# Performance work log

Measured on AMD Instinct MI355X. Metric: run time of the kernel, lower is better.

The kernel has to match this reference:

```python
import jax, jax.numpy as jnp
import numpy as np

N_NODES = 50000
N_EDGES = 800000
F_IN = 256
HID = 64
HEADS = 4
NEG_SLOPE = 0.2


def setup_inputs() -> dict:
    key = jax.random.key(0)
    ks = jax.random.split(key, 12)
    x = jax.random.normal(ks[0], (N_NODES, F_IN), dtype=jnp.float32)
    src = jax.random.randint(ks[1], (N_EDGES,), 0, N_NODES)
    dst = jax.random.randint(ks[2], (N_EDGES,), 0, N_NODES)
    s0 = 1.0 / np.sqrt(F_IN)
    s1 = 1.0 / np.sqrt(HEADS * HID)
    W0 = jax.random.normal(ks[3], (F_IN, HEADS * HID), dtype=jnp.float32) * s0
    a_l0 = jax.random.normal(ks[4], (HEADS, HID), dtype=jnp.float32) * s1
    a_r0 = jax.random.normal(ks[5], (HEADS, HID), dtype=jnp.float32) * s1
    b0 = jnp.zeros((HEADS * HID,), dtype=jnp.float32)
    W1 = jax.random.normal(ks[6], (HEADS * HID, HEADS * HID), dtype=jnp.float32) * s1
    a_l1 = jax.random.normal(ks[7], (HEADS, HID), dtype=jnp.float32) * s1
    a_r1 = jax.random.normal(ks[8], (HEADS, HID), dtype=jnp.float32) * s1
    b1 = jnp.zeros((HEADS * HID,), dtype=jnp.float32)
    return {"x": x, "src": src, "dst": dst,
            "W0": W0, "a_l0": a_l0, "a_r0": a_r0, "b0": b0,
            "W1": W1, "a_l1": a_l1, "a_r1": a_r1, "b1": b1}


def _gat_layer(h, src, dst, W, a_l, a_r, b):
    # h: [N, F_in] -> feat: [N, H, D]
    feat = (h @ W).reshape(h.shape[0], HEADS, HID)
    el = jnp.sum(feat * a_l, axis=-1)  # [N, H]
    er = jnp.sum(feat * a_r, axis=-1)  # [N, H]
    e = jax.nn.leaky_relu(el[src] + er[dst], NEG_SLOPE)  # [E, H]
    # per-destination edge softmax (numerically stable)
    m = jax.ops.segment_max(e, dst, num_segments=N_NODES)  # [N, H]
    ex = jnp.exp(e - m[dst])
    s = jax.ops.segment_sum(ex, dst, num_segments=N_NODES)  # [N, H]
    alpha = ex / jnp.maximum(s[dst], 1e-9)  # [E, H]
    msg = feat[src] * alpha[:, :, None]  # [E, H, D]
    rst = jax.ops.segment_sum(msg, dst, num_segments=N_NODES)  # [N, H, D]
    rst = rst + b.reshape(1, HEADS, HID)
    return jax.nn.elu(rst)


def reference(x, src, dst, W0, a_l0, a_r0, b0, W1, a_l1, a_r1, b1):
    h = _gat_layer(x, src, dst, W0, a_l0, a_r0, b0)  # [N, H, D]
    h = h.reshape(N_NODES, HEADS * HID)              # flatten(1)
    h = _gat_layer(h, src, dst, W1, a_l1, a_r1, b1)  # [N, H, D]
    # list of per-head outputs h[:, i]
    return tuple(h[:, i] for i in range(HEADS))
```

## Files before the change

kernel.cpp:

```cpp
#include <hip/hip_runtime.h>
#include <math.h>

#define N_NODES 50000
#define N_EDGES 800000
#define HEADS 4
#define HID 64
#define FDIM 256
#define SCAN_CHUNK 1024
#define SCAN_NB ((N_NODES + SCAN_CHUNK - 1) / SCAN_CHUNK)

typedef __attribute__((ext_vector_type(8))) _Float16 half8;
typedef __attribute__((ext_vector_type(4))) _Float16 half4;
typedef __attribute__((ext_vector_type(4))) float f32x4;

__device__ __forceinline__ void gload_lds16(const void* g, void* l) {
    __builtin_amdgcn_global_load_lds((const __attribute__((address_space(1))) void*)g,
                                     (__attribute__((address_space(3))) void*)l, 16, 0, 0);
}


__global__ __launch_bounds__(256) void scan_local(const int* __restrict__ counts,
                                                  int* __restrict__ offs,
                                                  int* __restrict__ bsum, int n) {
    __shared__ int part[256];
    const int b = blockIdx.x, t = threadIdx.x;
    const int base = b * SCAN_CHUNK + t * 4;
    int v[4];
#pragma unroll
    for (int j = 0; j < 4; j++) {
        int idx = base + j;
        v[j] = (idx < n) ? counts[idx] : 0;
    }
    int s0 = v[0], s1 = s0 + v[1], s2 = s1 + v[2], s3 = s2 + v[3];
    part[t] = s3;
    __syncthreads();
    for (int off = 1; off < 256; off <<= 1) {
        int x = (t >= off) ? part[t - off] : 0;
        __syncthreads();
        part[t] += x;
        __syncthreads();
    }
    int prefix = (t > 0) ? part[t - 1] : 0;
    int e[4] = {prefix, prefix + s0, prefix + s1, prefix + s2};
#pragma unroll
    for (int j = 0; j < 4; j++) {
        int idx = base + j;
        if (idx < n) offs[idx] = e[j];
    }
    if (t == 255) bsum[b] = part[255];
}

__global__ __launch_bounds__(64) void scan_bsum(int* __restrict__ bsum,
                                                int* __restrict__ offs, int nb, int n) {
    int lane = threadIdx.x;
    int own = (lane < nb) ? bsum[lane] : 0;
    int v = own;
    for (int off = 1; off < 64; off <<= 1) {
        int x = __shfl_up(v, off);
        if (lane >= off) v += x;
    }
    if (lane < nb) bsum[lane] = v - own;
    if (lane == nb - 1) offs[n] = v;
}

__global__ __launch_bounds__(256) void scan_add(int* __restrict__ offs,
                                                const int* __restrict__ bsum, int n) {
    const int b = blockIdx.x;
    const int p = bsum[b];
    const int base = b * SCAN_CHUNK + threadIdx.x * 4;
#pragma unroll
    for (int j = 0; j < 4; j++) {
        int idx = base + j;
        if (idx < n) offs[idx] += p;
    }
}

__global__ __launch_bounds__(256) void scatter_kernel(const int* __restrict__ src,
                                                      const int* __restrict__ dst,
                                                      const int* __restrict__ offs,
                                                      const int* __restrict__ rank,
                                                      int* __restrict__ csr_src, int E) {
    int i = blockIdx.x * blockDim.x + threadIdx.x;
    if (i < E) {
        int d = dst[i];
        csr_src[offs[d] + rank[i]] = src[i];
    }
}


__global__ __launch_bounds__(256) void wcast_kernel(const float* __restrict__ W0,
                                                    const float* __restrict__ W1,
                                                    _Float16* __restrict__ wt0,
                                                    _Float16* __restrict__ wt1) {
    const float* W = blockIdx.y ? W1 : W0;
    _Float16* wt = blockIdx.y ? wt1 : wt0;
    int n = blockIdx.x * 16 + (threadIdx.x >> 4);
    int k0 = (threadIdx.x & 15) * 16;
    for (int j = 0; j < 16; j++)
        wt[n * FDIM + k0 + j] = (_Float16)W[(k0 + j) * FDIM + n];
}

template <int A32, int DO_HIST>
__global__ __launch_bounds__(512) void mfma_gemm(const _Float16* __restrict__ A16,
                                                 const float* __restrict__ Af,
                                                 const _Float16* __restrict__ Bt,
                                                 const float* __restrict__ al,
                                                 const float* __restrict__ ar,
                                                 _Float16* __restrict__ feat16,
                                                 float* __restrict__ el,
                                                 float* __restrict__ er,
                                                 const int* __restrict__ dst,
                                                 int* __restrict__ counts,
                                                 int* __restrict__ rank) {
    __shared__ _Float16 ash[2][64 * 32];
    __shared__ _Float16 bsh[2][256 * 32];

    const int t = threadIdx.x;
    const int m0 = blockIdx.x * 64;
    const int wave = t >> 6, lane = t & 63;
    const int quad = lane >> 4, l16 = lane & 15;
    const int wr = (wave >> 2) * 32;
    const int wc = (wave & 3) * 64;

    const int arow = t >> 3, aq4 = t & 7;
    const int agr = (m0 + arow < N_NODES) ? m0 + arow : N_NODES - 1;
    const int aswz = (aq4 >> 1) ^ (arow & 3) ^ ((arow >> 2) & 3);
    const int aoff = arow * 32 + aswz * 8 + (aq4 & 1) * 4;

    const f32x4 zero = {0.f, 0.f, 0.f, 0.f};
    f32x4 acc[2][4];
#pragma unroll
    for (int i = 0; i < 2; i++)
#pragma unroll
        for (int j = 0; j < 4; j++) acc[i][j] = zero;

    const int rslot = (quad ^ (l16 & 3) ^ (l16 >> 2)) * 8;

    float4 areg;

    if (A32) {
        const float* p = &Af[(size_t)agr * FDIM + aq4 * 4];
        float4 f0 = *(const float4*)p;
        half4 hv = {(_Float16)f0.x, (_Float16)f0.y, (_Float16)f0.z, (_Float16)f0.w};
        *(half4*)&ash[0][aoff] = hv;
    } else {
        if (wave < 4) {
            int u = wave * 64 + lane;
            int row = u >> 2, sl = u & 3;
            int ss = sl ^ (row & 3) ^ ((row >> 2) & 3);
            int gr = (m0 + row < N_NODES) ? m0 + row : N_NODES - 1;
            gload_lds16(&A16[(size_t)gr * FDIM + ss * 8], &ash[0][u * 8]);
        }
    }
#pragma unroll
    for (int ii = 0; ii < 2; ii++) {
        int u = (wave * 2 + ii) * 64 + lane;
        int row = u >> 2, sl = u & 3;
        int ss = sl ^ (row & 3) ^ ((row >> 2) & 3);
        gload_lds16(&Bt[(size_t)row * FDIM + ss * 8], &bsh[0][u * 8]);
    }
    __syncthreads();

    for (int ks = 0; ks < 8; ks++) {
        const int cur = ks & 1, nxt = cur ^ 1;
        const int kk2 = (ks + 1) * 32;
        const bool pf = (ks < 7);

        if (pf) {
            if (A32) {
                areg = *(const float4*)&Af[(size_t)agr * FDIM + kk2 + aq4 * 4];
            } else {
                if (wave < 4) {
                    int u = wave * 64 + lane;
                    int row = u >> 2, sl = u & 3;
                    int ss = sl ^ (row & 3) ^ ((row >> 2) & 3);
                    int gr = (m0 + row < N_NODES) ? m0 + row : N_NODES - 1;
                    gload_lds16(&A16[(size_t)gr * FDIM + kk2 + ss * 8], &ash[nxt][u * 8]);
                }
            }
#pragma unroll
            for (int ii = 0; ii < 2; ii++) {
                int u = (wave * 2 + ii) * 64 + lane;
                int row = u >> 2, sl = u & 3;
                int ss = sl ^ (row & 3) ^ ((row >> 2) & 3);
                gload_lds16(&Bt[(size_t)row * FDIM + kk2 + ss * 8], &bsh[nxt][u * 8]);
            }
        }

        half8 af[2], bf[4];
#pragma unroll
        for (int i = 0; i < 2; i++)
            af[i] = *(half8*)&ash[cur][(wr + i * 16 + l16) * 32 + rslot];
#pragma unroll
        for (int i = 0; i < 4; i++)
            bf[i] = *(half8*)&bsh[cur][(wc + i * 16 + l16) * 32 + rslot];

#pragma unroll
        for (int mt = 0; mt < 2; mt++)
#pragma unroll
            for (int nt = 0; nt < 4; nt++)
                acc[mt][nt] = __builtin_amdgcn_mfma_f32_16x16x32_f16(bf[nt], af[mt], acc[mt][nt], 0, 0, 0);

        if (A32 && pf) {
            half4 hv = {(_Float16)areg.x, (_Float16)areg.y, (_Float16)areg.z, (_Float16)areg.w};
            *(half4*)&ash[nxt][aoff] = hv;
        }
        if (pf) __syncthreads();
    }

    if (DO_HIST) {
        for (int i = blockIdx.x * 512 + t; i < N_EDGES; i += gridDim.x * 512)
            rank[i] = atomicAdd(&counts[dst[i]], 1);
    }

    const int h = wc >> 6;
    float4 alv[4], arv[4];
#pragma unroll
    for (int nt = 0; nt < 4; nt++) {
        alv[nt] = *(const float4*)&al[wc + nt * 16 + quad * 4];
        arv[nt] = *(const float4*)&ar[wc + nt * 16 + quad * 4];
    }
#pragma unroll
    for (int mt = 0; mt < 2; mt++) {
        const int m = m0 + wr + mt * 16 + l16;
        const bool ok = (m < N_NODES);
        float pl = 0.f, pr = 0.f;
#pragma unroll
        for (int nt = 0; nt < 4; nt++) {
            f32x4 v = acc[mt][nt];
            if (ok) {
                half4 hv = {(_Float16)v[0], (_Float16)v[1], (_Float16)v[2], (_Float16)v[3]};
                *(half4*)&feat16[(size_t)m * FDIM + wc + nt * 16 + quad * 4] = hv;
            }
            pl += v[0] * alv[nt].x + v[1] * alv[nt].y + v[2] * alv[nt].z + v[3] * alv[nt].w;
            pr += v[0] * arv[nt].x + v[1] * arv[nt].y + v[2] * arv[nt].z + v[3] * arv[nt].w;
        }
        pl += __shfl_xor(pl, 16);
        pl += __shfl_xor(pl, 32);
        pr += __shfl_xor(pr, 16);
        pr += __shfl_xor(pr, 32);
        if (quad == 0 && ok) {
            el[m * 4 + h] = pl;
            er[m * 4 + h] = pr;
        }
    }
}

__global__ __launch_bounds__(256) void agg_fused(const _Float16* __restrict__ feat16,
                                                 const float* __restrict__ el,
                                                 const float* __restrict__ er,
                                                 const float* __restrict__ bias,
                                                 const int* __restrict__ offs,
                                                 const int* __restrict__ csr_src,
                                                 float* __restrict__ out,
                                                 _Float16* __restrict__ h1,
                                                 int mode) {
    const int wave = threadIdx.x >> 6;
    const int lane = threadIdx.x & 63;
    const int n = blockIdx.x * 4 + wave;
    const int head = lane >> 4;
    const int f = lane * 4;
    const int base16 = lane & 48;
    const int j16 = lane & 15;
    const int beg = offs[n];
    const int end = offs[n + 1];
    const float er_h = er[n * 4 + head];

    float4 acc = make_float4(0.f, 0.f, 0.f, 0.f);
    float ss = 0.f;

    for (int c = beg; c < end; c += 16) {
        int e = c + j16;
        int s_own = 0;
        float w_own = 0.f;
        if (e < end) {
            s_own = csr_src[e];
            float lg = el[s_own * 4 + head] + er_h;
            lg = (lg > 0.f) ? lg : 0.2f * lg;
            w_own = __expf(lg);
        }
        ss += w_own;

        int rem = end - c;
        if (rem > 16) rem = 16;

        int j = 0;
        for (; j + 3 < rem; j += 4) {
            int s0 = __shfl(s_own, base16 + j);
            int s1 = __shfl(s_own, base16 + j + 1);
            int s2 = __shfl(s_own, base16 + j + 2);
            int s3 = __shfl(s_own, base16 + j + 3);
            float w0 = __shfl(w_own, base16 + j);
            float w1 = __shfl(w_own, base16 + j + 1);
            float w2 = __shfl(w_own, base16 + j + 2);
            float w3 = __shfl(w_own, base16 + j + 3);
            half4 v0 = *(const half4*)&feat16[(size_t)s0 * FDIM + f];
            half4 v1 = *(const half4*)&feat16[(size_t)s1 * FDIM + f];
            half4 v2 = *(const half4*)&feat16[(size_t)s2 * FDIM + f];
            half4 v3 = *(const half4*)&feat16[(size_t)s3 * FDIM + f];
            acc.x += w0 * (float)v0[0] + w1 * (float)v1[0];
            acc.y += w0 * (float)v0[1] + w1 * (float)v1[1];
            acc.z += w0 * (float)v0[2] + w1 * (float)v1[2];
            acc.w += w0 * (float)v0[3] + w1 * (float)v1[3];
            acc.x += w2 * (float)v2[0] + w3 * (float)v3[0];
            acc.y += w2 * (float)v2[1] + w3 * (float)v3[1];
            acc.z += w2 * (float)v2[2] + w3 * (float)v3[2];
            acc.w += w2 * (float)v2[3] + w3 * (float)v3[3];
        }
        for (; j < rem; j++) {
            int s0 = __shfl(s_own, base16 + j);
            float w0 = __shfl(w_own, base16 + j);
            half4 v0 = *(const half4*)&feat16[(size_t)s0 * FDIM + f];
            acc.x += w0 * (float)v0[0];
            acc.y += w0 * (float)v0[1];
            acc.z += w0 * (float)v0[2];
            acc.w += w0 * (float)v0[3];
        }
    }

    ss += __shfl_xor(ss, 1, 16);
    ss += __shfl_xor(ss, 2, 16);
    ss += __shfl_xor(ss, 4, 16);
    ss += __shfl_xor(ss, 8, 16);

    float S = fmaxf(ss, 1e-9f);
    float inv = 1.f / S;
    float4 bv = *(const float4*)&bias[f];
    float r0 = acc.x * inv + bv.x;
    float r1 = acc.y * inv + bv.y;
    float r2 = acc.z * inv + bv.z;
    float r3 = acc.w * inv + bv.w;
    r0 = (r0 > 0.f) ? r0 : expm1f(r0);
    r1 = (r1 > 0.f) ? r1 : expm1f(r1);
    r2 = (r2 > 0.f) ? r2 : expm1f(r2);
    r3 = (r3 > 0.f) ? r3 : expm1f(r3);

    if (mode) {
        const int d = (lane & 15) * 4;
        float4 rv = make_float4(r0, r1, r2, r3);
        *(float4*)&out[(size_t)head * N_NODES * HID + (size_t)n * HID + d] = rv;
    } else {
        half4 hv = {(_Float16)r0, (_Float16)r1, (_Float16)r2, (_Float16)r3};
        *(half4*)&h1[(size_t)n * FDIM + f] = hv;
    }
}


extern "C" void kernel_launch(void* const* d_in, const int* in_sizes, int n_in,
                              void* d_out, int out_size, void* d_ws, size_t ws_size,
                              hipStream_t stream) {
    const float* x   = (const float*)d_in[0];
    const int*   src = (const int*)d_in[1];
    const int*   dst = (const int*)d_in[2];
    const float* W0  = (const float*)d_in[3];
    const float* al0 = (const float*)d_in[4];
    const float* ar0 = (const float*)d_in[5];
    const float* b0  = (const float*)d_in[6];
    const float* W1  = (const float*)d_in[7];
    const float* al1 = (const float*)d_in[8];
    const float* ar1 = (const float*)d_in[9];
    const float* b1  = (const float*)d_in[10];
    float* out = (float*)d_out;

    _Float16* h1 = (_Float16*)d_out;

    _Float16* feat16 = (_Float16*)d_ws;
    _Float16* wt0 = feat16 + (size_t)N_NODES * FDIM;
    _Float16* wt1 = wt0 + FDIM * FDIM;
    float* el    = (float*)(wt1 + FDIM * FDIM);
    float* er    = el + N_NODES * HEADS;
    int* counts  = (int*)(er + N_NODES * HEADS);
    int* offs    = counts + N_NODES;
    int* bsum    = offs + 50016;
    int* csr_src = bsum + 64;
    int* rank    = csr_src + N_EDGES;

    const int ggrid = (N_NODES + 63) / 64;

    hipMemsetAsync(counts, 0, N_NODES * sizeof(int), stream);
    wcast_kernel<<<dim3(16, 2), 256, 0, stream>>>(W0, W1, wt0, wt1);

    mfma_gemm<1, 1><<<ggrid, 512, 0, stream>>>(nullptr, x, wt0, al0, ar0,
                                               feat16, el, er, dst, counts, rank);

    scan_local<<<SCAN_NB, 256, 0, stream>>>(counts, offs, bsum, N_NODES);
    scan_bsum<<<1, 64, 0, stream>>>(bsum, offs, SCAN_NB, N_NODES);
    scan_add<<<SCAN_NB, 256, 0, stream>>>(offs, bsum, N_NODES);
    scatter_kernel<<<(N_EDGES + 255) / 256, 256, 0, stream>>>(src, dst, offs, rank, csr_src, N_EDGES);

    agg_fused<<<N_NODES / 4, 256, 0, stream>>>(feat16, el, er, b0, offs, csr_src,
                                               out, h1, 0);

    mfma_gemm<0, 0><<<ggrid, 512, 0, stream>>>(h1, nullptr, wt1, al1, ar1,
                                               feat16, el, er, nullptr, nullptr, nullptr);
    agg_fused<<<N_NODES / 4, 256, 0, stream>>>(feat16, el, er, b1, offs, csr_src,
                                               out, h1, 1);
}
```

Baseline: 343.7 us.

## Fuse weight cast with counter zeroing and use single-pass decoupled lookback scan

```diff
diff --git a/kernel.cpp b/kernel.cpp
--- a/kernel.cpp
+++ b/kernel.cpp
@@ -18,11 +18,36 @@
                                      (__attribute__((address_space(3))) void*)l, 16, 0, 0);
 }
 
-
-__global__ __launch_bounds__(256) void scan_local(const int* __restrict__ counts,
-                                                  int* __restrict__ offs,
-                                                  int* __restrict__ bsum, int n) {
+__global__ __launch_bounds__(256) void prep_kernel(const float* __restrict__ W0,
+                                                   const float* __restrict__ W1,
+                                                   _Float16* __restrict__ wt0,
+                                                   _Float16* __restrict__ wt1,
+                                                   int* __restrict__ counts,
+                                                   int* __restrict__ flags) {
+    const int b = blockIdx.x, t = threadIdx.x;
+    if (b < 32) {
+        const float* W = (b >= 16) ? W1 : W0;
+        _Float16* wt = (b >= 16) ? wt1 : wt0;
+        int n = (b & 15) * 16 + (t >> 4);
+        int k0 = (t & 15) * 16;
+        for (int j = 0; j < 16; j++)
+            wt[n * FDIM + k0 + j] = (_Float16)W[(k0 + j) * FDIM + n];
+    } else {
+        int4 z = make_int4(0, 0, 0, 0);
+        int4* p = (int4*)counts;
+        for (int k = (b - 32) * 256 + t; k < N_NODES / 4; k += 13 * 256)
+            p[k] = z;
+        if (b == 32 && t < 64) flags[t] = 0;
+    }
+}
+
+__global__ __launch_bounds__(256) void scan_lookback(const int* __restrict__ counts,
+                                                     int* __restrict__ offs,
+                                                     int* __restrict__ aggv,
+                                                     int* __restrict__ prefv,
+                                                     int* __restrict__ flags, int n) {
     __shared__ int part[256];
+    __shared__ int sh_exc;
     const int b = blockIdx.x, t = threadIdx.x;
     const int base = b * SCAN_CHUNK + t * 4;
     int v[4];
@@ -40,39 +65,40 @@
         part[t] += x;
         __syncthreads();
     }
-    int prefix = (t > 0) ? part[t - 1] : 0;
+    const int total = part[255];
+
+    if (t == 0) {
+        atomicExch(&aggv[b], total);
+        __threadfence();
+        atomicExch(&flags[b], 1);
+    }
+    if (t < 64) {
+        int p = b - 1 - t;
+        int f = 2, a = 0;
+        if (p >= 0) {
+            do { f = atomicAdd(&flags[p], 0); } while (f == 0);
+            a = (f == 2) ? atomicAdd(&prefv[p], 0) : atomicAdd(&aggv[p], 0);
+        }
+        unsigned long long m = __ballot(f == 2);
+        int t2 = __ffsll((long long)m) - 1;
+        int contrib = (t <= t2) ? a : 0;
+        for (int off = 32; off; off >>= 1) contrib += __shfl_down(contrib, off);
+        if (t == 0) {
+            atomicExch(&prefv[b], contrib + total);
+            __threadfence();
+            atomicExch(&flags[b], 2);
+            sh_exc = contrib;
+        }
+    }
+    __syncthreads();
+    const int prefix = sh_exc + ((t > 0) ? part[t - 1] : 0);
     int e[4] = {prefix, prefix + s0, prefix + s1, prefix + s2};
 #pragma unroll
     for (int j = 0; j < 4; j++) {
         int idx = base + j;
         if (idx < n) offs[idx] = e[j];
     }
-    if (t == 255) bsum[b] = part[255];
-}
-
-__global__ __launch_bounds__(64) void scan_bsum(int* __restrict__ bsum,
-                                                int* __restrict__ offs, int nb, int n) {
-    int lane = threadIdx.x;
-    int own = (lane < nb) ? bsum[lane] : 0;
-    int v = own;
-    for (int off = 1; off < 64; off <<= 1) {
-        int x = __shfl_up(v, off);
-        if (lane >= off) v += x;
-    }
-    if (lane < nb) bsum[lane] = v - own;
-    if (lane == nb - 1) offs[n] = v;
-}
-
-__global__ __launch_bounds__(256) void scan_add(int* __restrict__ offs,
-                                                const int* __restrict__ bsum, int n) {
-    const int b = blockIdx.x;
-    const int p = bsum[b];
-    const int base = b * SCAN_CHUNK + threadIdx.x * 4;
-#pragma unroll
-    for (int j = 0; j < 4; j++) {
-        int idx = base + j;
-        if (idx < n) offs[idx] += p;
-    }
+    if (b == (int)gridDim.x - 1 && t == 255) offs[n] = sh_exc + total;
 }
 
 __global__ __launch_bounds__(256) void scatter_kernel(const int* __restrict__ src,
@@ -85,19 +111,6 @@
         int d = dst[i];
         csr_src[offs[d] + rank[i]] = src[i];
     }
-}
-
-
-__global__ __launch_bounds__(256) void wcast_kernel(const float* __restrict__ W0,
-                                                    const float* __restrict__ W1,
-                                                    _Float16* __restrict__ wt0,
-                                                    _Float16* __restrict__ wt1) {
-    const float* W = blockIdx.y ? W1 : W0;
-    _Float16* wt = blockIdx.y ? wt1 : wt0;
-    int n = blockIdx.x * 16 + (threadIdx.x >> 4);
-    int k0 = (threadIdx.x & 15) * 16;
-    for (int j = 0; j < 16; j++)
-        wt[n * FDIM + k0 + j] = (_Float16)W[(k0 + j) * FDIM + n];
 }
 
 template <int A32, int DO_HIST>
@@ -371,21 +384,20 @@
     float* er    = el + N_NODES * HEADS;
     int* counts  = (int*)(er + N_NODES * HEADS);
     int* offs    = counts + N_NODES;
-    int* bsum    = offs + 50016;
-    int* csr_src = bsum + 64;
+    int* aggv    = offs + 50016;
+    int* prefv   = aggv + 64;
+    int* flags   = prefv + 64;
+    int* csr_src = flags + 64;
     int* rank    = csr_src + N_EDGES;
 
     const int ggrid = (N_NODES + 63) / 64;
 
-    hipMemsetAsync(counts, 0, N_NODES * sizeof(int), stream);
-    wcast_kernel<<<dim3(16, 2), 256, 0, stream>>>(W0, W1, wt0, wt1);
+    prep_kernel<<<45, 256, 0, stream>>>(W0, W1, wt0, wt1, counts, flags);
 
     mfma_gemm<1, 1><<<ggrid, 512, 0, stream>>>(nullptr, x, wt0, al0, ar0,
                                                feat16, el, er, dst, counts, rank);
 
-    scan_local<<<SCAN_NB, 256, 0, stream>>>(counts, offs, bsum, N_NODES);
-    scan_bsum<<<1, 64, 0, stream>>>(bsum, offs, SCAN_NB, N_NODES);
-    scan_add<<<SCAN_NB, 256, 0, stream>>>(offs, bsum, N_NODES);
+    scan_lookback<<<SCAN_NB, 256, 0, stream>>>(counts, offs, aggv, prefv, flags, N_NODES);
     scatter_kernel<<<(N_EDGES + 255) / 256, 256, 0, stream>>>(src, dst, offs, rank, csr_src, N_EDGES);
 
     agg_fused<<<N_NODES / 4, 256, 0, stream>>>(feat16, el, er, b0, offs, csr_src,
```

After: 334.5 us. -2.7%, faster.
